# Optimization experiments

Measured on AMD Instinct MI355X. Metric: run time of the kernel, lower is better.

## Reference

```python
import jax, jax.numpy as jnp
import numpy as np

BS, L, D = 32, 512, 512
N_CHARS = 32
DICT = 97

def setup_inputs() -> dict:
    key = jax.random.key(0)
    ks = jax.random.split(key, 10)
    s = 1.0 / np.sqrt(D)
    return {
        "inp": jax.random.normal(ks[0], (BS, L, D), jnp.float32),
        "emb": jax.random.normal(ks[1], (N_CHARS, D), jnp.float32) * 0.02,  # embedding table; char_orders == arange
        "Wo_w": jax.random.normal(ks[2], (D, D), jnp.float32) * s,
        "Wo_b": jnp.zeros((D,), jnp.float32),
        "Wv_w": jax.random.normal(ks[3], (D, D), jnp.float32) * s,
        "Wv_b": jnp.zeros((D,), jnp.float32),
        "We_w": jax.random.normal(ks[4], (D, 1), jnp.float32) * s,
        "We_b": jnp.zeros((1,), jnp.float32),
        "Wc_w": jax.random.normal(ks[5], (D, DICT), jnp.float32) * s,
        "Wc_b": jnp.zeros((DICT,), jnp.float32),
    }

def reference(inp, emb, Wo_w, Wo_b, Wv_w, Wv_b, We_w, We_b, Wc_w, Wc_b):
    # O = embedding(arange(max_n_chars)) is just the full embedding table: (n, d)
    w_o = emb @ Wo_w + Wo_b                      # (n, d)
    w_v = inp @ Wv_w + Wv_b                      # (b, L, d)
    # broadcast add -> tanh -> score projection: (b, n, L, d) -> (b, n, L)
    h = jnp.tanh(w_o[None, :, None, :] + w_v[:, None, :, :])
    e = jnp.einsum('bnld,d->bnl', h, We_w[:, 0]) + We_b[0]
    alpha = jax.nn.softmax(e, axis=2)            # softmax over L (axis=2)
    visual_features = jnp.einsum('bnl,bld->bnd', alpha, inp)  # (b, n, d)
    logits = visual_features @ Wc_w + Wc_b       # (b, n, dict)
    return (visual_features, logits)
```

## Files before the change

kernel.cpp:

```cpp
#include <hip/hip_runtime.h>
#include <hip/hip_bf16.h>

#define BS    32
#define LSEQ  512
#define DIM   512
#define NCH   32
#define NDICT 97
#define CHB   16

#define TANH_SCALE 2.8853900817779268f

typedef __attribute__((ext_vector_type(8))) short bf16x8;
typedef __attribute__((ext_vector_type(4))) float f32x4;

#define GLDS16(gsrc, ldst) \
  __builtin_amdgcn_global_load_lds((const __attribute__((address_space(1))) void*)(gsrc), \
                                   (__attribute__((address_space(3))) void*)(ldst), 16, 0, 0)

__device__ __forceinline__ float sig_from_scaled(float xs) {
    float e2 = __builtin_amdgcn_exp2f(xs);
    return __builtin_amdgcn_rcpf(1.0f + e2);
}

__device__ __forceinline__ void split2u(float x0, float x1, unsigned& hp, unsigned& lp) {
    unsigned r0 = __float_as_uint(x0) + 0x8000u;
    unsigned r1 = __float_as_uint(x1) + 0x8000u;
    float f0 = __uint_as_float(r0 & 0xFFFF0000u);
    float f1 = __uint_as_float(r1 & 0xFFFF0000u);
    hp = (r0 >> 16) | (r1 & 0xFFFF0000u);
    unsigned s0 = __float_as_uint(x0 - f0);
    unsigned s1 = __float_as_uint(x1 - f1);
    lp = (s0 >> 16) | (s1 & 0xFFFF0000u);
}

__global__ __launch_bounds__(256) void k_prep(
    const float* __restrict__ Wv, ushort* __restrict__ BhiT, ushort* __restrict__ BloT,
    const float* __restrict__ Wo, ushort* __restrict__ WohiT, ushort* __restrict__ WoloT,
    const float* __restrict__ emb, ushort* __restrict__ embH, ushort* __restrict__ embL)
{
    __shared__ float tile[64][65];
    const int bid = blockIdx.x;
    const int t = threadIdx.x;
    if (bid < 128) {
        const bool isWv = bid < 64;
        const float* src = isWv ? Wv : Wo;
        ushort* dH = isWv ? BhiT : WohiT;
        ushort* dL = isWv ? BloT : WoloT;
        const int bb = bid & 63;
        const int k0 = (bb >> 3) * 64, n0 = (bb & 7) * 64;
        const int tr = t >> 4, tc = (t & 15) * 4;
        #pragma unroll
        for (int rr = 0; rr < 64; rr += 16) {
            float4 v = *(const float4*)&src[(size_t)(k0 + rr + tr) * DIM + n0 + tc];
            tile[rr + tr][tc + 0] = v.x; tile[rr + tr][tc + 1] = v.y;
            tile[rr + tr][tc + 2] = v.z; tile[rr + tr][tc + 3] = v.w;
        }
        __syncthreads();
        #pragma unroll
        for (int rr = 0; rr < 64; rr += 16) {
            const int n = rr + tr;
            unsigned h01, l01, h23, l23;
            split2u(tile[tc + 0][n] * TANH_SCALE, tile[tc + 1][n] * TANH_SCALE, h01, l01);
            split2u(tile[tc + 2][n] * TANH_SCALE, tile[tc + 3][n] * TANH_SCALE, h23, l23);
            *(uint2*)&dH[(size_t)(n0 + n) * DIM + k0 + tc] = make_uint2(h01, h23);
            *(uint2*)&dL[(size_t)(n0 + n) * DIM + k0 + tc] = make_uint2(l01, l23);
        }
    } else {
        for (int i = t; i < 4096; i += 256) {
            float4 v = ((const float4*)emb)[i];
            unsigned h01, l01, h23, l23;
            split2u(v.x, v.y, h01, l01);
            split2u(v.z, v.w, h23, l23);
            ((uint2*)embH)[i] = make_uint2(h01, h23);
            ((uint2*)embL)[i] = make_uint2(l01, l23);
        }
    }
}

__global__ __launch_bounds__(256) void k_gemm(
    const float* __restrict__ A,
    const ushort* __restrict__ Bhi, const ushort* __restrict__ Blo,
    const float* __restrict__ bias, float* __restrict__ C,
    const ushort* __restrict__ WohiT, const ushort* __restrict__ WoloT,
    const ushort* __restrict__ embH, const ushort* __restrict__ embL,
    const float* __restrict__ Wo_b, float* __restrict__ w_o)
{
    __shared__ float  AfS[2 * 128 * 32];
    __shared__ ushort BhS[2 * 128 * 32];
    __shared__ ushort BlS[2 * 128 * 32];

    const int bid = blockIdx.x;
    const int t = threadIdx.x;
    const int wave = t >> 6, lane = t & 63;

    const int sgB = (lane & 3) ^ ((lane >> 3) & 3);
    const int sgA = (lane & 7) ^ ((lane >> 3) & 7);

    const int fr   = lane & 15;
    const int q    = lane >> 4;
    const int fswzB = (q ^ ((fr >> 1) & 3)) * 8;

    if (bid < 512) {
        const int mb = (bid & 7) * 16 + (bid >> 5);
        const int nb = (bid >> 3) & 3;
        const int bm = mb * 128, bn = nb * 128;
        const int wm = wave >> 1, wn = wave & 1;
        const int brow0 = (wn * 64 + fr) * 32;
        const int pA0 = (2 * q) ^ (fr & 7);
        const int pA1 = (2 * q + 1) ^ (fr & 7);

        f32x4 acc[4][4] = {};

        auto stage = [&](int p, int k0) {
            #pragma unroll
            for (int c4 = 0; c4 < 4; ++c4) {
                const int ca = wave * 4 + c4;
                const size_t ga = (size_t)(bm + ca * 8 + (lane >> 3)) * DIM + k0 + sgA * 4;
                GLDS16(A + ga, &AfS[p * 4096 + ca * 256]);
                const int idx = wave * 4 + c4;
                const int pl = idx & 1, cb = idx >> 1;
                const size_t gb = (size_t)(bn + cb * 16 + (lane >> 2)) * DIM + k0 + sgB * 8;
                if (pl) { GLDS16(Blo + gb, &BlS[p * 4096 + cb * 512]); }
                else    { GLDS16(Bhi + gb, &BhS[p * 4096 + cb * 512]); }
            }
        };

        stage(0, 0);
        __syncthreads();
        int cur = 0;
        for (int ks = 0; ks < 16; ++ks) {
            if (ks < 15) stage(cur ^ 1, (ks + 1) * 32);
            const int co = cur * 4096;
            bf16x8 ah[4], al[4], bh[4], bl[4];
            #pragma unroll
            for (int i = 0; i < 4; ++i) {
                const float* arow = &AfS[co + (wm * 64 + i * 16 + fr) * 32];
                float4 fa = *(const float4*)&arow[pA0 * 4];
                float4 fb = *(const float4*)&arow[pA1 * 4];
                union { unsigned u[4]; bf16x8 v; } H, L;
                split2u(fa.x, fa.y, H.u[0], L.u[0]);
                split2u(fa.z, fa.w, H.u[1], L.u[1]);
                split2u(fb.x, fb.y, H.u[2], L.u[2]);
                split2u(fb.z, fb.w, H.u[3], L.u[3]);
                ah[i] = H.v; al[i] = L.v;
                bh[i] = *(const bf16x8*)&BhS[co + brow0 + i * 512 + fswzB];
                bl[i] = *(const bf16x8*)&BlS[co + brow0 + i * 512 + fswzB];
            }
            #pragma unroll
            for (int i = 0; i < 4; ++i)
                #pragma unroll
                for (int j = 0; j < 4; ++j) {
                    acc[i][j] = __builtin_amdgcn_mfma_f32_16x16x32_bf16(ah[i], bh[j], acc[i][j], 0, 0, 0);
                    acc[i][j] = __builtin_amdgcn_mfma_f32_16x16x32_bf16(ah[i], bl[j], acc[i][j], 0, 0, 0);
                    acc[i][j] = __builtin_amdgcn_mfma_f32_16x16x32_bf16(al[i], bh[j], acc[i][j], 0, 0, 0);
                }
            __syncthreads();
            cur ^= 1;
        }

        #pragma unroll
        for (int i = 0; i < 4; ++i) {
            const int m = bm + wm * 64 + i * 16 + q * 4;
            #pragma unroll
            for (int j = 0; j < 4; ++j) {
                const int n = bn + wn * 64 + j * 16 + fr;
                const float bb = TANH_SCALE * bias[n];
                #pragma unroll
                for (int r = 0; r < 4; ++r)
                    C[(size_t)(m + r) * DIM + n] = acc[i][j][r] + bb;
            }
        }
    } else {
        const int nb0 = (bid - 512) * 128;
        const int crow0 = (wave * 32 + fr) * 32;
        f32x4 acc[2][2] = {};

        for (int k0 = 0; k0 < DIM; k0 += 32) {
            #pragma unroll
            for (int c4 = 0; c4 < 4; ++c4) {
                const int idx = wave * 4 + c4;
                const int pl = idx & 1, c = idx >> 1;
                const size_t gb = (size_t)(nb0 + c * 16 + (lane >> 2)) * DIM + k0 + sgB * 8;
                if (pl) { GLDS16(WoloT + gb, &BlS[c * 512]); }
                else    { GLDS16(WohiT + gb, &BhS[c * 512]); }
            }
            bf16x8 eh[2], el[2];
            #pragma unroll
            for (int m = 0; m < 2; ++m) {
                const size_t ra = (size_t)(m * 16 + fr) * DIM + k0 + q * 8;
                eh[m] = *(const bf16x8*)&embH[ra];
                el[m] = *(const bf16x8*)&embL[ra];
            }
            __syncthreads();

            bf16x8 bh[2], bl[2];
            #pragma unroll
            for (int j = 0; j < 2; ++j) {
                bh[j] = *(const bf16x8*)&BhS[crow0 + j * 512 + fswzB];
                bl[j] = *(const bf16x8*)&BlS[crow0 + j * 512 + fswzB];
            }
            #pragma unroll
            for (int m = 0; m < 2; ++m)
                #pragma unroll
                for (int j = 0; j < 2; ++j) {
                    acc[m][j] = __builtin_amdgcn_mfma_f32_16x16x32_bf16(eh[m], bh[j], acc[m][j], 0, 0, 0);
                    acc[m][j] = __builtin_amdgcn_mfma_f32_16x16x32_bf16(eh[m], bl[j], acc[m][j], 0, 0, 0);
                    acc[m][j] = __builtin_amdgcn_mfma_f32_16x16x32_bf16(el[m], bh[j], acc[m][j], 0, 0, 0);
                }
            __syncthreads();
        }

        #pragma unroll
        for (int m = 0; m < 2; ++m) {
            const int row = m * 16 + q * 4;
            #pragma unroll
            for (int j = 0; j < 2; ++j) {
                const int col = nb0 + wave * 32 + j * 16 + fr;
                const float bb = TANH_SCALE * Wo_b[col];
                #pragma unroll
                for (int r = 0; r < 4; ++r)
                    w_o[(size_t)(row + r) * DIM + col] = acc[m][j][r] + bb;
            }
        }
    }
}

__global__ __launch_bounds__(256, 4) void k_e(
    const float* __restrict__ w_v, const float* __restrict__ w_o,
    const float* __restrict__ We_w, float* __restrict__ e)
{
    __shared__ float4 woS[CHB * 128];
    const int lblk = blockIdx.x;
    const int b    = blockIdx.y;
    const int ch0  = blockIdx.z * CHB;
    const int t    = threadIdx.x;

    const float4* wog = ((const float4*)w_o) + ch0 * (DIM / 4);
    #pragma unroll
    for (int i = 0; i < CHB * 128 / 256; ++i)
        woS[t + 256 * i] = wog[t + 256 * i];

    const int wave = t >> 6, lane = t & 63;
    const int g = lane >> 4, j = lane & 15;
    const int l = lblk * 16 + wave * 4 + g;

    const float4* wvp = (const float4*)(w_v + (size_t)(b * LSEQ + l) * DIM);
    const float4* wep = (const float4*)We_w;
    float4 wv[8], we[8];
    #pragma unroll
    for (int k = 0; k < 8; ++k) {
        wv[k] = wvp[16 * k + j];
        we[k] = wep[16 * k + j];
    }
    float wsum = 0.0f;
    #pragma unroll
    for (int k = 0; k < 8; ++k)
        wsum += (we[k].x + we[k].y) + (we[k].z + we[k].w);
    #pragma unroll
    for (int off = 1; off < 16; off <<= 1) wsum += __shfl_xor(wsum, off, 64);

    __syncthreads();

    float sv[CHB];
    #pragma unroll 4
    for (int i = 0; i < CHB; ++i) {
        const float4* wrow = &woS[i * 128];
        float s0 = 0.f, s1 = 0.f, s2 = 0.f, s3 = 0.f;
        #pragma unroll
        for (int k = 0; k < 8; ++k) {
            float4 wo4 = wrow[16 * k + j];
            s0 = fmaf(we[k].x, sig_from_scaled(wo4.x + wv[k].x), s0);
            s1 = fmaf(we[k].y, sig_from_scaled(wo4.y + wv[k].y), s1);
            s2 = fmaf(we[k].z, sig_from_scaled(wo4.z + wv[k].z), s2);
            s3 = fmaf(we[k].w, sig_from_scaled(wo4.w + wv[k].w), s3);
        }
        sv[i] = (s0 + s1) + (s2 + s3);
    }

    float t2[8];
    #pragma unroll
    for (int i = 0; i < 8; ++i) {
        float a = sv[2 * i]     + __shfl_xor(sv[2 * i],     1, 64);
        float c = sv[2 * i + 1] + __shfl_xor(sv[2 * i + 1], 1, 64);
        t2[i] = (j & 1) ? c : a;
    }
    float t4[4];
    #pragma unroll
    for (int i = 0; i < 4; ++i) {
        float a = t2[2 * i]     + __shfl_xor(t2[2 * i],     2, 64);
        float c = t2[2 * i + 1] + __shfl_xor(t2[2 * i + 1], 2, 64);
        t4[i] = (j & 2) ? c : a;
    }
    float t8[2];
    #pragma unroll
    for (int i = 0; i < 2; ++i) {
        float a = t4[2 * i]     + __shfl_xor(t4[2 * i],     4, 64);
        float c = t4[2 * i + 1] + __shfl_xor(t4[2 * i + 1], 4, 64);
        t8[i] = (j & 4) ? c : a;
    }
    float a = t8[0] + __shfl_xor(t8[0], 8, 64);
    float c = t8[1] + __shfl_xor(t8[1], 8, 64);
    float res = (j & 8) ? c : a;

    e[(size_t)(b * NCH + ch0 + j) * LSEQ + l] = fmaf(-2.0f, res, wsum);
}

__global__ __launch_bounds__(256) void k_soft(
    const float* __restrict__ e, ushort* __restrict__ aH, ushort* __restrict__ aL)
{
    const int row = blockIdx.x * 4 + (threadIdx.x >> 6);
    const int lane = threadIdx.x & 63;
    const float4* erow = (const float4*)(e + (size_t)row * LSEQ);
    float4 v0 = erow[2 * lane], v1 = erow[2 * lane + 1];
    float m = fmaxf(fmaxf(fmaxf(v0.x, v0.y), fmaxf(v0.z, v0.w)),
                    fmaxf(fmaxf(v1.x, v1.y), fmaxf(v1.z, v1.w)));
    #pragma unroll
    for (int off = 32; off > 0; off >>= 1) m = fmaxf(m, __shfl_xor(m, off, 64));
    float p[8];
    p[0] = __expf(v0.x - m); p[1] = __expf(v0.y - m);
    p[2] = __expf(v0.z - m); p[3] = __expf(v0.w - m);
    p[4] = __expf(v1.x - m); p[5] = __expf(v1.y - m);
    p[6] = __expf(v1.z - m); p[7] = __expf(v1.w - m);
    float s = ((p[0] + p[1]) + (p[2] + p[3])) + ((p[4] + p[5]) + (p[6] + p[7]));
    #pragma unroll
    for (int off = 32; off > 0; off >>= 1) s += __shfl_xor(s, off, 64);
    const float inv = 1.0f / s;
    unsigned h01, l01, h23, l23, h45, l45, h67, l67;
    split2u(p[0] * inv, p[1] * inv, h01, l01);
    split2u(p[2] * inv, p[3] * inv, h23, l23);
    split2u(p[4] * inv, p[5] * inv, h45, l45);
    split2u(p[6] * inv, p[7] * inv, h67, l67);
    uint2* oh = (uint2*)(aH + (size_t)row * LSEQ);
    uint2* ol = (uint2*)(aL + (size_t)row * LSEQ);
    oh[2 * lane]     = make_uint2(h01, h23);
    oh[2 * lane + 1] = make_uint2(h45, h67);
    ol[2 * lane]     = make_uint2(l01, l23);
    ol[2 * lane + 1] = make_uint2(l45, l67);
}

__global__ __launch_bounds__(256) void k_vf(
    const float* __restrict__ inp,
    const ushort* __restrict__ aH, const ushort* __restrict__ aL,
    float* __restrict__ part)
{
    __shared__ unsigned T[4][16 * 68];
    const int dgrp = blockIdx.x >> 1, ls = blockIdx.x & 1;
    const int b = blockIdx.y;
    const int t = threadIdx.x, wave = t >> 6, lane = t & 63;
    const int d0 = (dgrp * 4 + wave) * 16;
    const int lbase = ls * 256;
    const int c = lane & 15, g = lane >> 4;

    unsigned* Tw = T[wave];
    const ushort* aHb = aH + (size_t)b * NCH * LSEQ;
    const ushort* aLb = aL + (size_t)b * NCH * LSEQ;

    f32x4 acc0 = {}, acc1 = {};

    for (int l0 = 0; l0 < 256; l0 += 64) {
        const float4* src = (const float4*)(inp + ((size_t)(b * LSEQ) + lbase + l0 + lane) * DIM + d0);
        float4 v0 = src[0], v1 = src[1], v2 = src[2], v3 = src[3];
        unsigned ev[16];
        {
            unsigned hp, lp;
            split2u(v0.x, v0.y, hp, lp); ev[0] = (lp << 16) | (hp & 0xFFFFu); ev[1] = (lp & 0xFFFF0000u) | (hp >> 16);
            split2u(v0.z, v0.w, hp, lp); ev[2] = (lp << 16) | (hp & 0xFFFFu); ev[3] = (lp & 0xFFFF0000u) | (hp >> 16);
            split2u(v1.x, v1.y, hp, lp); ev[4] = (lp << 16) | (hp & 0xFFFFu); ev[5] = (lp & 0xFFFF0000u) | (hp >> 16);
            split2u(v1.z, v1.w, hp, lp); ev[6] = (lp << 16) | (hp & 0xFFFFu); ev[7] = (lp & 0xFFFF0000u) | (hp >> 16);
            split2u(v2.x, v2.y, hp, lp); ev[8] = (lp << 16) | (hp & 0xFFFFu); ev[9] = (lp & 0xFFFF0000u) | (hp >> 16);
            split2u(v2.z, v2.w, hp, lp); ev[10] = (lp << 16) | (hp & 0xFFFFu); ev[11] = (lp & 0xFFFF0000u) | (hp >> 16);
            split2u(v3.x, v3.y, hp, lp); ev[12] = (lp << 16) | (hp & 0xFFFFu); ev[13] = (lp & 0xFFFF0000u) | (hp >> 16);
            split2u(v3.z, v3.w, hp, lp); ev[14] = (lp << 16) | (hp & 0xFFFFu); ev[15] = (lp & 0xFFFF0000u) | (hp >> 16);
        }
        #pragma unroll
        for (int i = 0; i < 16; ++i)
            Tw[i * 68 + lane] = ev[i];
        #pragma unroll
        for (int ks = 0; ks < 2; ++ks) {
            const unsigned* bp = &Tw[c * 68 + ks * 32 + g * 8];
            uint4 w0 = *(const uint4*)bp;
            uint4 w1 = *(const uint4*)(bp + 4);
            union { unsigned u[4]; bf16x8 v; } H, L;
            H.u[0] = (w0.x & 0xFFFFu) | (w0.y << 16);
            H.u[1] = (w0.z & 0xFFFFu) | (w0.w << 16);
            H.u[2] = (w1.x & 0xFFFFu) | (w1.y << 16);
            H.u[3] = (w1.z & 0xFFFFu) | (w1.w << 16);
            L.u[0] = (w0.x >> 16) | (w0.y & 0xFFFF0000u);
            L.u[1] = (w0.z >> 16) | (w0.w & 0xFFFF0000u);
            L.u[2] = (w1.x >> 16) | (w1.y & 0xFFFF0000u);
            L.u[3] = (w1.z >> 16) | (w1.w & 0xFFFF0000u);

            const int lfrag = lbase + l0 + ks * 32 + g * 8;
            bf16x8 a0h = *(const bf16x8*)&aHb[(size_t)c * LSEQ + lfrag];
            bf16x8 a0l = *(const bf16x8*)&aLb[(size_t)c * LSEQ + lfrag];
            bf16x8 a1h = *(const bf16x8*)&aHb[(size_t)(16 + c) * LSEQ + lfrag];
            bf16x8 a1l = *(const bf16x8*)&aLb[(size_t)(16 + c) * LSEQ + lfrag];

            acc0 = __builtin_amdgcn_mfma_f32_16x16x32_bf16(a0h, H.v, acc0, 0, 0, 0);
            acc0 = __builtin_amdgcn_mfma_f32_16x16x32_bf16(a0h, L.v, acc0, 0, 0, 0);
            acc0 = __builtin_amdgcn_mfma_f32_16x16x32_bf16(a0l, H.v, acc0, 0, 0, 0);
            acc1 = __builtin_amdgcn_mfma_f32_16x16x32_bf16(a1h, H.v, acc1, 0, 0, 0);
            acc1 = __builtin_amdgcn_mfma_f32_16x16x32_bf16(a1h, L.v, acc1, 0, 0, 0);
            acc1 = __builtin_amdgcn_mfma_f32_16x16x32_bf16(a1l, H.v, acc1, 0, 0, 0);
        }
    }

    const size_t base = (size_t)(ls * BS * NCH + b * NCH) * DIM + d0 + c;
    #pragma unroll
    for (int r = 0; r < 4; ++r) {
        part[base + (size_t)(g * 4 + r) * DIM]        = acc0[r];
        part[base + (size_t)(16 + g * 4 + r) * DIM]   = acc1[r];
    }
}

__global__ __launch_bounds__(256) void k_lg(
    const float* __restrict__ part, const float* __restrict__ Wc_w,
    const float* __restrict__ Wc_b, float* __restrict__ out_vf,
    float* __restrict__ out_logits)
{
    __shared__ float vfS[4][DIM];
    __shared__ float lgS[2][4][NDICT];
    const int r0 = blockIdx.x * 4;
    const int t = threadIdx.x;
    const int wave = t >> 6, lane = t & 63;

    const float2* p0 = (const float2*)(part + (size_t)(r0 + wave) * DIM);
    const float2* p1 = (const float2*)(part + (size_t)(BS * NCH + r0 + wave) * DIM);
    float2* vout = (float2*)(out_vf + (size_t)(r0 + wave) * DIM);
    #pragma unroll
    for (int q = 0; q < 4; ++q) {
        float2 x = p0[lane + 64 * q], y = p1[lane + 64 * q];
        float2 z; z.x = x.x + y.x; z.y = x.y + y.y;
        ((float2*)&vfS[wave][0])[lane + 64 * q] = z;
        vout[lane + 64 * q] = z;
    }
    __syncthreads();

    const int j = t & 127, half = t >> 7;
    if (j < NDICT) {
        const float* wc = Wc_w + (size_t)half * 256 * NDICT + j;
        const float* v0 = &vfS[0][half * 256];
        const float* v1 = &vfS[1][half * 256];
        const float* v2 = &vfS[2][half * 256];
        const float* v3 = &vfS[3][half * 256];
        float a0 = 0.f, a1 = 0.f, a2 = 0.f, a3 = 0.f;
        #pragma unroll 4
        for (int d = 0; d < 256; ++d) {
            float w = wc[(size_t)d * NDICT];
            a0 = fmaf(v0[d], w, a0); a1 = fmaf(v1[d], w, a1);
            a2 = fmaf(v2[d], w, a2); a3 = fmaf(v3[d], w, a3);
        }
        lgS[half][0][j] = a0; lgS[half][1][j] = a1;
        lgS[half][2][j] = a2; lgS[half][3][j] = a3;
    }
    __syncthreads();
    for (int idx = t; idx < 4 * NDICT; idx += 256) {
        const int r = idx / NDICT, jj = idx - r * NDICT;
        out_logits[(size_t)(r0 + r) * NDICT + jj] = Wc_b[jj] + lgS[0][r][jj] + lgS[1][r][jj];
    }
}

extern "C" void kernel_launch(void* const* d_in, const int* in_sizes, int n_in,
                              void* d_out, int out_size, void* d_ws, size_t ws_size,
                              hipStream_t stream)
{
    const float* inp  = (const float*)d_in[0];
    const float* emb  = (const float*)d_in[1];
    const float* Wo_w = (const float*)d_in[2];
    const float* Wo_b = (const float*)d_in[3];
    const float* Wv_w = (const float*)d_in[4];
    const float* Wv_b = (const float*)d_in[5];
    const float* We_w = (const float*)d_in[6];
    const float* Wc_w = (const float*)d_in[8];
    const float* Wc_b = (const float*)d_in[9];

    char* p = (char*)d_ws;
    float*  w_o   = (float*)p;  p += (64 << 10);
    float*  ev    = (float*)p;  p += (size_t)BS * NCH * LSEQ * 4;
    ushort* BhiT  = (ushort*)p; p += (size_t)DIM * DIM * 2;
    ushort* BloT  = (ushort*)p; p += (size_t)DIM * DIM * 2;
    ushort* WohiT = (ushort*)p; p += (size_t)DIM * DIM * 2;
    ushort* WoloT = (ushort*)p; p += (size_t)DIM * DIM * 2;
    ushort* embH  = (ushort*)p; p += (size_t)NCH * DIM * 2;
    ushort* embL  = (ushort*)p; p += (size_t)NCH * DIM * 2;
    ushort* aH    = (ushort*)p; p += (size_t)BS * NCH * LSEQ * 2;
    ushort* aL    = (ushort*)p; p += (size_t)BS * NCH * LSEQ * 2;
    float*  partV = (float*)p;  p += (size_t)2 * BS * NCH * DIM * 4;
    float*  w_v   = (float*)p;

    float* out_vf = (float*)d_out;
    float* out_lg = out_vf + BS * NCH * DIM;

    k_prep<<<dim3(129), dim3(256), 0, stream>>>(Wv_w, BhiT, BloT, Wo_w, WohiT, WoloT,
                                                emb, embH, embL);
    k_gemm<<<dim3(516), dim3(256), 0, stream>>>(inp, BhiT, BloT, Wv_b, w_v,
                                                WohiT, WoloT, embH, embL, Wo_b, w_o);
    k_e<<<dim3(LSEQ / 16, BS, NCH / CHB), dim3(256), 0, stream>>>(w_v, w_o, We_w, ev);
    k_soft<<<dim3(256), dim3(256), 0, stream>>>(ev, aH, aL);
    k_vf<<<dim3(16, BS), dim3(256), 0, stream>>>(inp, aH, aL, partV);
    k_lg<<<dim3(256), dim3(256), 0, stream>>>(partV, Wc_w, Wc_b, out_vf, out_lg);
}
```

Before: 144.0 us.

## Fuse score computation into w_v GEMM epilogue with per-N-block partial sums

```diff
diff --git a/kernel.cpp b/kernel.cpp
--- a/kernel.cpp
+++ b/kernel.cpp
@@ -6,7 +6,6 @@
 #define DIM   512
 #define NCH   32
 #define NDICT 97
-#define CHB   16
 
 #define TANH_SCALE 2.8853900817779268f
 
@@ -31,6 +30,41 @@
     unsigned s0 = __float_as_uint(x0 - f0);
     unsigned s1 = __float_as_uint(x1 - f1);
     lp = (s0 >> 16) | (s1 & 0xFFFF0000u);
+}
+
+__device__ __forceinline__ float sig4(float4 wo, float4 wv, float4 we, float s) {
+    s = fmaf(we.x, sig_from_scaled(wo.x + wv.x), s);
+    s = fmaf(we.y, sig_from_scaled(wo.y + wv.y), s);
+    s = fmaf(we.z, sig_from_scaled(wo.z + wv.z), s);
+    s = fmaf(we.w, sig_from_scaled(wo.w + wv.w), s);
+    return s;
+}
+
+__device__ __forceinline__ float tree16(const float* sv, int j) {
+    float t2[8];
+    #pragma unroll
+    for (int i = 0; i < 8; ++i) {
+        float a = sv[2 * i]     + __shfl_xor(sv[2 * i],     1, 64);
+        float c = sv[2 * i + 1] + __shfl_xor(sv[2 * i + 1], 1, 64);
+        t2[i] = (j & 1) ? c : a;
+    }
+    float t4[4];
+    #pragma unroll
+    for (int i = 0; i < 4; ++i) {
+        float a = t2[2 * i]     + __shfl_xor(t2[2 * i],     2, 64);
+        float c = t2[2 * i + 1] + __shfl_xor(t2[2 * i + 1], 2, 64);
+        t4[i] = (j & 2) ? c : a;
+    }
+    float t8[2];
+    #pragma unroll
+    for (int i = 0; i < 2; ++i) {
+        float a = t4[2 * i]     + __shfl_xor(t4[2 * i],     4, 64);
+        float c = t4[2 * i + 1] + __shfl_xor(t4[2 * i + 1], 4, 64);
+        t8[i] = (j & 4) ? c : a;
+    }
+    float a = t8[0] + __shfl_xor(t8[0], 8, 64);
+    float c = t8[1] + __shfl_xor(t8[1], 8, 64);
+    return (j & 8) ? c : a;
 }
 
 __global__ __launch_bounds__(256) void k_prep(
@@ -77,17 +111,82 @@
     }
 }
 
-__global__ __launch_bounds__(256) void k_gemm(
-    const float* __restrict__ A,
-    const ushort* __restrict__ Bhi, const ushort* __restrict__ Blo,
-    const float* __restrict__ bias, float* __restrict__ C,
+__global__ __launch_bounds__(256) void k_wo(
     const ushort* __restrict__ WohiT, const ushort* __restrict__ WoloT,
     const ushort* __restrict__ embH, const ushort* __restrict__ embL,
     const float* __restrict__ Wo_b, float* __restrict__ w_o)
 {
-    __shared__ float  AfS[2 * 128 * 32];
-    __shared__ ushort BhS[2 * 128 * 32];
-    __shared__ ushort BlS[2 * 128 * 32];
+    __shared__ ushort BhS[4096], BlS[4096];
+    const int t = threadIdx.x;
+    const int wave = t >> 6, lane = t & 63;
+    const int sgB = (lane & 3) ^ ((lane >> 3) & 3);
+    const int fr = lane & 15;
+    const int q  = lane >> 4;
+    const int fswzB = (q ^ ((fr >> 1) & 3)) * 8;
+    const int nb0 = blockIdx.x * 128;
+    const int crow0 = (wave * 32 + fr) * 32;
+    f32x4 acc[2][2] = {};
+
+    for (int k0 = 0; k0 < DIM; k0 += 32) {
+        #pragma unroll
+        for (int c4 = 0; c4 < 4; ++c4) {
+            const int idx = wave * 4 + c4;
+            const int pl = idx & 1, c = idx >> 1;
+            const size_t gb = (size_t)(nb0 + c * 16 + (lane >> 2)) * DIM + k0 + sgB * 8;
+            if (pl) { GLDS16(WoloT + gb, &BlS[c * 512]); }
+            else    { GLDS16(WohiT + gb, &BhS[c * 512]); }
+        }
+        bf16x8 eh[2], el[2];
+        #pragma unroll
+        for (int m = 0; m < 2; ++m) {
+            const size_t ra = (size_t)(m * 16 + fr) * DIM + k0 + q * 8;
+            eh[m] = *(const bf16x8*)&embH[ra];
+            el[m] = *(const bf16x8*)&embL[ra];
+        }
+        __syncthreads();
+        bf16x8 bh[2], bl[2];
+        #pragma unroll
+        for (int j = 0; j < 2; ++j) {
+            bh[j] = *(const bf16x8*)&BhS[crow0 + j * 512 + fswzB];
+            bl[j] = *(const bf16x8*)&BlS[crow0 + j * 512 + fswzB];
+        }
+        #pragma unroll
+        for (int m = 0; m < 2; ++m)
+            #pragma unroll
+            for (int j = 0; j < 2; ++j) {
+                acc[m][j] = __builtin_amdgcn_mfma_f32_16x16x32_bf16(eh[m], bh[j], acc[m][j], 0, 0, 0);
+                acc[m][j] = __builtin_amdgcn_mfma_f32_16x16x32_bf16(eh[m], bl[j], acc[m][j], 0, 0, 0);
+                acc[m][j] = __builtin_amdgcn_mfma_f32_16x16x32_bf16(el[m], bh[j], acc[m][j], 0, 0, 0);
+            }
+        __syncthreads();
+    }
+    #pragma unroll
+    for (int m = 0; m < 2; ++m) {
+        const int row = m * 16 + q * 4;
+        #pragma unroll
+        for (int j = 0; j < 2; ++j) {
+            const int col = nb0 + wave * 32 + j * 16 + fr;
+            const float bb = TANH_SCALE * Wo_b[col];
+            #pragma unroll
+            for (int r = 0; r < 4; ++r)
+                w_o[(size_t)(row + r) * DIM + col] = acc[m][j][r] + bb;
+        }
+    }
+}
+
+__global__ __launch_bounds__(256) void k_gemm_e(
+    const float* __restrict__ A,
+    const ushort* __restrict__ Bhi, const ushort* __restrict__ Blo,
+    const float* __restrict__ bias,
+    const float* __restrict__ w_o, const float* __restrict__ We_w,
+    float* __restrict__ partial)
+{
+    __shared__ __align__(16) char smem[65536];
+    float*  AfS = (float*)smem;
+    ushort* BhS = (ushort*)(smem + 32768);
+    ushort* BlS = (ushort*)(smem + 49152);
+    float*  woS = (float*)smem;
+    float*  wvS = (float*)(smem + 16384);
 
     const int bid = blockIdx.x;
     const int t = threadIdx.x;
@@ -95,227 +194,152 @@
 
     const int sgB = (lane & 3) ^ ((lane >> 3) & 3);
     const int sgA = (lane & 7) ^ ((lane >> 3) & 7);
-
-    const int fr   = lane & 15;
-    const int q    = lane >> 4;
+    const int fr = lane & 15;
+    const int q  = lane >> 4;
     const int fswzB = (q ^ ((fr >> 1) & 3)) * 8;
 
-    if (bid < 512) {
-        const int mb = (bid & 7) * 16 + (bid >> 5);
-        const int nb = (bid >> 3) & 3;
-        const int bm = mb * 128, bn = nb * 128;
-        const int wm = wave >> 1, wn = wave & 1;
-        const int brow0 = (wn * 64 + fr) * 32;
-        const int pA0 = (2 * q) ^ (fr & 7);
-        const int pA1 = (2 * q + 1) ^ (fr & 7);
-
-        f32x4 acc[4][4] = {};
-
-        auto stage = [&](int p, int k0) {
+    const int mb = (bid & 7) * 16 + (bid >> 5);
+    const int nb = (bid >> 3) & 3;
+    const int bm = mb * 128, bn = nb * 128;
+    const int wm = wave >> 1, wn = wave & 1;
+    const int brow0 = (wn * 64 + fr) * 32;
+    const int pA0 = (2 * q) ^ (fr & 7);
+    const int pA1 = (2 * q + 1) ^ (fr & 7);
+
+    f32x4 acc[4][4] = {};
+
+    auto stage = [&](int p, int k0) {
+        #pragma unroll
+        for (int c4 = 0; c4 < 4; ++c4) {
+            const int ca = wave * 4 + c4;
+            const size_t ga = (size_t)(bm + ca * 8 + (lane >> 3)) * DIM + k0 + sgA * 4;
+            GLDS16(A + ga, &AfS[p * 4096 + ca * 256]);
+            const int pl = ca & 1, cb = ca >> 1;
+            const size_t gb = (size_t)(bn + cb * 16 + (lane >> 2)) * DIM + k0 + sgB * 8;
+            if (pl) { GLDS16(Blo + gb, &BlS[p * 4096 + cb * 512]); }
+            else    { GLDS16(Bhi + gb, &BhS[p * 4096 + cb * 512]); }
+        }
+    };
+
+    stage(0, 0);
+    __syncthreads();
+    int cur = 0;
+    for (int ks = 0; ks < 16; ++ks) {
+        if (ks < 15) stage(cur ^ 1, (ks + 1) * 32);
+        const int co = cur * 4096;
+        bf16x8 ah[4], al[4], bh[4], bl[4];
+        #pragma unroll
+        for (int i = 0; i < 4; ++i) {
+            const float* arow = &AfS[co + (wm * 64 + i * 16 + fr) * 32];
+            float4 fa = *(const float4*)&arow[pA0 * 4];
+            float4 fb = *(const float4*)&arow[pA1 * 4];
+            union { unsigned u[4]; bf16x8 v; } H, L;
+            split2u(fa.x, fa.y, H.u[0], L.u[0]);
+            split2u(fa.z, fa.w, H.u[1], L.u[1]);
+            split2u(fb.x, fb.y, H.u[2], L.u[2]);
+            split2u(fb.z, fb.w, H.u[3], L.u[3]);
+            ah[i] = H.v; al[i] = L.v;
+            bh[i] = *(const bf16x8*)&BhS[co + brow0 + i * 512 + fswzB];
+            bl[i] = *(const bf16x8*)&BlS[co + brow0 + i * 512 + fswzB];
+        }
+        #pragma unroll
+        for (int i = 0; i < 4; ++i)
             #pragma unroll
-            for (int c4 = 0; c4 < 4; ++c4) {
-                const int ca = wave * 4 + c4;
-                const size_t ga = (size_t)(bm + ca * 8 + (lane >> 3)) * DIM + k0 + sgA * 4;
-                GLDS16(A + ga, &AfS[p * 4096 + ca * 256]);
-                const int idx = wave * 4 + c4;
-                const int pl = idx & 1, cb = idx >> 1;
-                const size_t gb = (size_t)(bn + cb * 16 + (lane >> 2)) * DIM + k0 + sgB * 8;
-                if (pl) { GLDS16(Blo + gb, &BlS[p * 4096 + cb * 512]); }
-                else    { GLDS16(Bhi + gb, &BhS[p * 4096 + cb * 512]); }
+            for (int j = 0; j < 4; ++j) {
+                acc[i][j] = __builtin_amdgcn_mfma_f32_16x16x32_bf16(ah[i], bh[j], acc[i][j], 0, 0, 0);
+                acc[i][j] = __builtin_amdgcn_mfma_f32_16x16x32_bf16(ah[i], bl[j], acc[i][j], 0, 0, 0);
+                acc[i][j] = __builtin_amdgcn_mfma_f32_16x16x32_bf16(al[i], bh[j], acc[i][j], 0, 0, 0);
             }
-        };
-
-        stage(0, 0);
         __syncthreads();
-        int cur = 0;
-        for (int ks = 0; ks < 16; ++ks) {
-            if (ks < 15) stage(cur ^ 1, (ks + 1) * 32);
-            const int co = cur * 4096;
-            bf16x8 ah[4], al[4], bh[4], bl[4];
-            #pragma unroll
-            for (int i = 0; i < 4; ++i) {
-                const float* arow = &AfS[co + (wm * 64 + i * 16 + fr) * 32];
-                float4 fa = *(const float4*)&arow[pA0 * 4];
-                float4 fb = *(const float4*)&arow[pA1 * 4];
-                union { unsigned u[4]; bf16x8 v; } H, L;
-                split2u(fa.x, fa.y, H.u[0], L.u[0]);
-                split2u(fa.z, fa.w, H.u[1], L.u[1]);
-                split2u(fb.x, fb.y, H.u[2], L.u[2]);
-                split2u(fb.z, fb.w, H.u[3], L.u[3]);
-                ah[i] = H.v; al[i] = L.v;
-                bh[i] = *(const bf16x8*)&BhS[co + brow0 + i * 512 + fswzB];
-                bl[i] = *(const bf16x8*)&BlS[co + brow0 + i * 512 + fswzB];
-            }
+        cur ^= 1;
+    }
+
+    #pragma unroll
+    for (int cc = 0; cc < 4; ++cc) {
+        const int flat = cc * 256 + t;
+        const float* src = w_o + (size_t)(flat >> 5) * DIM + bn + ((flat & 31) << 2);
+        GLDS16(src, &woS[cc * 1024 + wave * 256]);
+    }
+
+    const float4* weP = (const float4*)(We_w + bn);
+    const float4 we0 = weP[fr];
+    const float4 we1 = weP[16 + fr];
+    float bb[4];
+    #pragma unroll
+    for (int jj = 0; jj < 4; ++jj)
+        bb[jj] = TANH_SCALE * bias[bn + wn * 64 + jj * 16 + fr];
+
+    const int b  = mb >> 2;
+    const int lb = (mb & 3) * 128;
+    float* part = partial + (size_t)nb * (BS * NCH * LSEQ);
+
+    #pragma unroll
+    for (int h = 0; h < 2; ++h) {
+        __syncthreads();
+        if (wm == h) {
             #pragma unroll
             for (int i = 0; i < 4; ++i)
                 #pragma unroll
-                for (int j = 0; j < 4; ++j) {
-                    acc[i][j] = __builtin_amdgcn_mfma_f32_16x16x32_bf16(ah[i], bh[j], acc[i][j], 0, 0, 0);
-                    acc[i][j] = __builtin_amdgcn_mfma_f32_16x16x32_bf16(ah[i], bl[j], acc[i][j], 0, 0, 0);
-                    acc[i][j] = __builtin_amdgcn_mfma_f32_16x16x32_bf16(al[i], bh[j], acc[i][j], 0, 0, 0);
-                }
-            __syncthreads();
-            cur ^= 1;
-        }
-
-        #pragma unroll
-        for (int i = 0; i < 4; ++i) {
-            const int m = bm + wm * 64 + i * 16 + q * 4;
-            #pragma unroll
-            for (int j = 0; j < 4; ++j) {
-                const int n = bn + wn * 64 + j * 16 + fr;
-                const float bb = TANH_SCALE * bias[n];
-                #pragma unroll
-                for (int r = 0; r < 4; ++r)
-                    C[(size_t)(m + r) * DIM + n] = acc[i][j][r] + bb;
+                for (int jj = 0; jj < 4; ++jj)
+                    #pragma unroll
+                    for (int r = 0; r < 4; ++r)
+                        wvS[(i * 16 + q * 4 + r) * 132 + wn * 64 + jj * 16 + fr] =
+                            acc[i][jj][r] + bb[jj];
+        }
+        __syncthreads();
+        for (int lp = 0; lp < 4; ++lp) {
+            const int lloc = wave * 16 + lp * 4 + q;
+            const float4* wvp4 = (const float4*)&wvS[lloc * 132];
+            const float4 wv0 = wvp4[fr];
+            const float4 wv1 = wvp4[16 + fr];
+            float sv0[16], sv1[16];
+            #pragma unroll 4
+            for (int ch = 0; ch < 16; ++ch) {
+                const float4* worow = (const float4*)&woS[ch * 128];
+                sv0[ch] = sig4(worow[16 + fr], wv1, we1, sig4(worow[fr], wv0, we0, 0.0f));
             }
-        }
-    } else {
-        const int nb0 = (bid - 512) * 128;
-        const int crow0 = (wave * 32 + fr) * 32;
-        f32x4 acc[2][2] = {};
-
-        for (int k0 = 0; k0 < DIM; k0 += 32) {
-            #pragma unroll
-            for (int c4 = 0; c4 < 4; ++c4) {
-                const int idx = wave * 4 + c4;
-                const int pl = idx & 1, c = idx >> 1;
-                const size_t gb = (size_t)(nb0 + c * 16 + (lane >> 2)) * DIM + k0 + sgB * 8;
-                if (pl) { GLDS16(WoloT + gb, &BlS[c * 512]); }
-                else    { GLDS16(WohiT + gb, &BhS[c * 512]); }
+            #pragma unroll 4
+            for (int ch = 0; ch < 16; ++ch) {
+                const float4* worow = (const float4*)&woS[(16 + ch) * 128];
+                sv1[ch] = sig4(worow[16 + fr], wv1, we1, sig4(worow[fr], wv0, we0, 0.0f));
             }
-            bf16x8 eh[2], el[2];
-            #pragma unroll
-            for (int m = 0; m < 2; ++m) {
-                const size_t ra = (size_t)(m * 16 + fr) * DIM + k0 + q * 8;
-                eh[m] = *(const bf16x8*)&embH[ra];
-                el[m] = *(const bf16x8*)&embL[ra];
-            }
-            __syncthreads();
-
-            bf16x8 bh[2], bl[2];
-            #pragma unroll
-            for (int j = 0; j < 2; ++j) {
-                bh[j] = *(const bf16x8*)&BhS[crow0 + j * 512 + fswzB];
-                bl[j] = *(const bf16x8*)&BlS[crow0 + j * 512 + fswzB];
-            }
-            #pragma unroll
-            for (int m = 0; m < 2; ++m)
-                #pragma unroll
-                for (int j = 0; j < 2; ++j) {
-                    acc[m][j] = __builtin_amdgcn_mfma_f32_16x16x32_bf16(eh[m], bh[j], acc[m][j], 0, 0, 0);
-                    acc[m][j] = __builtin_amdgcn_mfma_f32_16x16x32_bf16(eh[m], bl[j], acc[m][j], 0, 0, 0);
-                    acc[m][j] = __builtin_amdgcn_mfma_f32_16x16x32_bf16(el[m], bh[j], acc[m][j], 0, 0, 0);
-                }
-            __syncthreads();
-        }
-
-        #pragma unroll
-        for (int m = 0; m < 2; ++m) {
-            const int row = m * 16 + q * 4;
-            #pragma unroll
-            for (int j = 0; j < 2; ++j) {
-                const int col = nb0 + wave * 32 + j * 16 + fr;
-                const float bb = TANH_SCALE * Wo_b[col];
-                #pragma unroll
-                for (int r = 0; r < 4; ++r)
-                    w_o[(size_t)(row + r) * DIM + col] = acc[m][j][r] + bb;
-            }
-        }
-    }
-}
-
-__global__ __launch_bounds__(256, 4) void k_e(
-    const float* __restrict__ w_v, const float* __restrict__ w_o,
-    const float* __restrict__ We_w, float* __restrict__ e)
-{
-    __shared__ float4 woS[CHB * 128];
-    const int lblk = blockIdx.x;
-    const int b    = blockIdx.y;
-    const int ch0  = blockIdx.z * CHB;
-    const int t    = threadIdx.x;
-
-    const float4* wog = ((const float4*)w_o) + ch0 * (DIM / 4);
-    #pragma unroll
-    for (int i = 0; i < CHB * 128 / 256; ++i)
-        woS[t + 256 * i] = wog[t + 256 * i];
-
-    const int wave = t >> 6, lane = t & 63;
-    const int g = lane >> 4, j = lane & 15;
-    const int l = lblk * 16 + wave * 4 + g;
-
-    const float4* wvp = (const float4*)(w_v + (size_t)(b * LSEQ + l) * DIM);
-    const float4* wep = (const float4*)We_w;
-    float4 wv[8], we[8];
-    #pragma unroll
-    for (int k = 0; k < 8; ++k) {
-        wv[k] = wvp[16 * k + j];
-        we[k] = wep[16 * k + j];
-    }
-    float wsum = 0.0f;
-    #pragma unroll
-    for (int k = 0; k < 8; ++k)
-        wsum += (we[k].x + we[k].y) + (we[k].z + we[k].w);
-    #pragma unroll
-    for (int off = 1; off < 16; off <<= 1) wsum += __shfl_xor(wsum, off, 64);
-
-    __syncthreads();
-
-    float sv[CHB];
-    #pragma unroll 4
-    for (int i = 0; i < CHB; ++i) {
-        const float4* wrow = &woS[i * 128];
-        float s0 = 0.f, s1 = 0.f, s2 = 0.f, s3 = 0.f;
-        #pragma unroll
-        for (int k = 0; k < 8; ++k) {
-            float4 wo4 = wrow[16 * k + j];
-            s0 = fmaf(we[k].x, sig_from_scaled(wo4.x + wv[k].x), s0);
-            s1 = fmaf(we[k].y, sig_from_scaled(wo4.y + wv[k].y), s1);
-            s2 = fmaf(we[k].z, sig_from_scaled(wo4.z + wv[k].z), s2);
-            s3 = fmaf(we[k].w, sig_from_scaled(wo4.w + wv[k].w), s3);
-        }
-        sv[i] = (s0 + s1) + (s2 + s3);
-    }
-
-    float t2[8];
-    #pragma unroll
-    for (int i = 0; i < 8; ++i) {
-        float a = sv[2 * i]     + __shfl_xor(sv[2 * i],     1, 64);
-        float c = sv[2 * i + 1] + __shfl_xor(sv[2 * i + 1], 1, 64);
-        t2[i] = (j & 1) ? c : a;
-    }
-    float t4[4];
-    #pragma unroll
-    for (int i = 0; i < 4; ++i) {
-        float a = t2[2 * i]     + __shfl_xor(t2[2 * i],     2, 64);
-        float c = t2[2 * i + 1] + __shfl_xor(t2[2 * i + 1], 2, 64);
-        t4[i] = (j & 2) ? c : a;
-    }
-    float t8[2];
-    #pragma unroll
-    for (int i = 0; i < 2; ++i) {
-        float a = t4[2 * i]     + __shfl_xor(t4[2 * i],     4, 64);
-        float c = t4[2 * i + 1] + __shfl_xor(t4[2 * i + 1], 4, 64);
-        t8[i] = (j & 4) ? c : a;
-    }
-    float a = t8[0] + __shfl_xor(t8[0], 8, 64);
-    float c = t8[1] + __shfl_xor(t8[1], 8, 64);
-    float res = (j & 8) ? c : a;
-
-    e[(size_t)(b * NCH + ch0 + j) * LSEQ + l] = fmaf(-2.0f, res, wsum);
+            const float res0 = tree16(sv0, fr);
+            const float res1 = tree16(sv1, fr);
+            const int lg = lb + h * 64 + lloc;
+            part[(size_t)(b * NCH + fr) * LSEQ + lg]      = res0;
+            part[(size_t)(b * NCH + 16 + fr) * LSEQ + lg] = res1;
+        }
+    }
 }
 
 __global__ __launch_bounds__(256) void k_soft(
-    const float* __restrict__ e, ushort* __restrict__ aH, ushort* __restrict__ aL)
+    const float* __restrict__ part, ushort* __restrict__ aH, ushort* __restrict__ aL)
 {
     const int row = blockIdx.x * 4 + (threadIdx.x >> 6);
     const int lane = threadIdx.x & 63;
-    const float4* erow = (const float4*)(e + (size_t)row * LSEQ);
-    float4 v0 = erow[2 * lane], v1 = erow[2 * lane + 1];
+    const size_t off = (size_t)row * LSEQ;
+    const size_t stride = (size_t)BS * NCH * LSEQ;
+    const float4* p0 = (const float4*)(part + off);
+    const float4* p1 = (const float4*)(part + stride + off);
+    const float4* p2 = (const float4*)(part + 2 * stride + off);
+    const float4* p3 = (const float4*)(part + 3 * stride + off);
+
+    float4 a0 = p0[2 * lane], a1 = p1[2 * lane], a2 = p2[2 * lane], a3 = p3[2 * lane];
+    float4 b0 = p0[2 * lane + 1], b1 = p1[2 * lane + 1], b2 = p2[2 * lane + 1], b3 = p3[2 * lane + 1];
+    float4 v0, v1;
+    v0.x = -2.0f * (((a0.x + a1.x) + (a2.x + a3.x)));
+    v0.y = -2.0f * (((a0.y + a1.y) + (a2.y + a3.y)));
+    v0.z = -2.0f * (((a0.z + a1.z) + (a2.z + a3.z)));
+    v0.w = -2.0f * (((a0.w + a1.w) + (a2.w + a3.w)));
+    v1.x = -2.0f * (((b0.x + b1.x) + (b2.x + b3.x)));
+    v1.y = -2.0f * (((b0.y + b1.y) + (b2.y + b3.y)));
+    v1.z = -2.0f * (((b0.z + b1.z) + (b2.z + b3.z)));
+    v1.w = -2.0f * (((b0.w + b1.w) + (b2.w + b3.w)));
+
     float m = fmaxf(fmaxf(fmaxf(v0.x, v0.y), fmaxf(v0.z, v0.w)),
                     fmaxf(fmaxf(v1.x, v1.y), fmaxf(v1.z, v1.w)));
     #pragma unroll
-    for (int off = 32; off > 0; off >>= 1) m = fmaxf(m, __shfl_xor(m, off, 64));
+    for (int offx = 32; offx > 0; offx >>= 1) m = fmaxf(m, __shfl_xor(m, offx, 64));
     float p[8];
     p[0] = __expf(v0.x - m); p[1] = __expf(v0.y - m);
     p[2] = __expf(v0.z - m); p[3] = __expf(v0.w - m);
@@ -323,7 +347,7 @@
     p[6] = __expf(v1.z - m); p[7] = __expf(v1.w - m);
     float s = ((p[0] + p[1]) + (p[2] + p[3])) + ((p[4] + p[5]) + (p[6] + p[7]));
     #pragma unroll
-    for (int off = 32; off > 0; off >>= 1) s += __shfl_xor(s, off, 64);
+    for (int offx = 32; offx > 0; offx >>= 1) s += __shfl_xor(s, offx, 64);
     const float inv = 1.0f / s;
     unsigned h01, l01, h23, l23, h45, l45, h67, l67;
     split2u(p[0] * inv, p[1] * inv, h01, l01);
@@ -428,11 +452,11 @@
     const float2* p1 = (const float2*)(part + (size_t)(BS * NCH + r0 + wave) * DIM);
     float2* vout = (float2*)(out_vf + (size_t)(r0 + wave) * DIM);
     #pragma unroll
-    for (int q = 0; q < 4; ++q) {
-        float2 x = p0[lane + 64 * q], y = p1[lane + 64 * q];
+    for (int qq = 0; qq < 4; ++qq) {
+        float2 x = p0[lane + 64 * qq], y = p1[lane + 64 * qq];
         float2 z; z.x = x.x + y.x; z.y = x.y + y.y;
-        ((float2*)&vfS[wave][0])[lane + 64 * q] = z;
-        vout[lane + 64 * q] = z;
+        ((float2*)&vfS[wave][0])[lane + 64 * qq] = z;
+        vout[lane + 64 * qq] = z;
     }
     __syncthreads();
 
@@ -476,7 +500,6 @@
 
     char* p = (char*)d_ws;
     float*  w_o   = (float*)p;  p += (64 << 10);
-    float*  ev    = (float*)p;  p += (size_t)BS * NCH * LSEQ * 4;
     ushort* BhiT  = (ushort*)p; p += (size_t)DIM * DIM * 2;
     ushort* BloT  = (ushort*)p; p += (size_t)DIM * DIM * 2;
     ushort* WohiT = (ushort*)p; p += (size_t)DIM * DIM * 2;
@@ -486,17 +509,16 @@
     ushort* aH    = (ushort*)p; p += (size_t)BS * NCH * LSEQ * 2;
     ushort* aL    = (ushort*)p; p += (size_t)BS * NCH * LSEQ * 2;
     float*  partV = (float*)p;  p += (size_t)2 * BS * NCH * DIM * 4;
-    float*  w_v   = (float*)p;
+    float*  partE = (float*)p;  p += (size_t)4 * BS * NCH * LSEQ * 4;
 
     float* out_vf = (float*)d_out;
     float* out_lg = out_vf + BS * NCH * DIM;
 
     k_prep<<<dim3(129), dim3(256), 0, stream>>>(Wv_w, BhiT, BloT, Wo_w, WohiT, WoloT,
                                                 emb, embH, embL);
-    k_gemm<<<dim3(516), dim3(256), 0, stream>>>(inp, BhiT, BloT, Wv_b, w_v,
-                                                WohiT, WoloT, embH, embL, Wo_b, w_o);
-    k_e<<<dim3(LSEQ / 16, BS, NCH / CHB), dim3(256), 0, stream>>>(w_v, w_o, We_w, ev);
-    k_soft<<<dim3(256), dim3(256), 0, stream>>>(ev, aH, aL);
+    k_wo<<<dim3(4), dim3(256), 0, stream>>>(WohiT, WoloT, embH, embL, Wo_b, w_o);
+    k_gemm_e<<<dim3(512), dim3(256), 0, stream>>>(inp, BhiT, BloT, Wv_b, w_o, We_w, partE);
+    k_soft<<<dim3(256), dim3(256), 0, stream>>>(partE, aH, aL);
     k_vf<<<dim3(16, BS), dim3(256), 0, stream>>>(inp, aH, aL, partV);
     k_lg<<<dim3(256), dim3(256), 0, stream>>>(partV, Wc_w, Wc_b, out_vf, out_lg);
 }
```

Measured after the change: 156.5 us. 1.09x slower.
